# Performance work log

Hardware: AMD Instinct MI355X
Metric: run time of the kernel (lower is better)

Reference implementation:

```python
import jax, jax.numpy as jnp
import numpy as np

D_K = 64

def setup_inputs() -> dict:
    key = jax.random.key(0)
    k1, k2, k3 = jax.random.split(key, 3)
    B, H, S, d = 4, 16, 2048, D_K
    Q = jax.random.normal(k1, (B, H, S, d), dtype=jnp.float32)
    K = jax.random.normal(k2, (B, H, S, d), dtype=jnp.float32)
    V = jax.random.normal(k3, (B, H, S, d), dtype=jnp.float32)
    attn_mask = jnp.ones((1, 1, S, S), dtype=jnp.float32)
    return {"Q": Q, "K": K, "V": V, "attn_mask": attn_mask}

def reference(Q, K, V, attn_mask):
    # scores = Q K^T / sqrt(d_k)  -> [B, H, S, S]
    scale = 1.0 / np.sqrt(D_K).astype(np.float32)
    scores = jnp.einsum('bhqd,bhkd->bhqk', Q, K) * scale
    # unnormalized exp (NO max-subtraction, faithful to original)
    scores = jnp.exp(scores)
    # multiplicative mask applied POST-exp
    scores = scores * attn_mask
    # manual sum-normalization with eps
    attn = scores / (jnp.sum(scores, axis=-1, keepdims=True) + 1e-08)
    context = jnp.einsum('bhqk,bhkd->bhqd', attn, V)
    return (context, attn)
```

## Files before the change

kernel.cpp:

```cpp
#include <hip/hip_runtime.h>

#define S_LEN 2048
#define D_KD  64
#define NKT   32
#define NBH   64
#define KSEG  4

typedef __attribute__((ext_vector_type(8))) short short8;
typedef __attribute__((ext_vector_type(4))) float f32x4;

__device__ __forceinline__ unsigned short f2bf(float f) {
    unsigned u = __builtin_bit_cast(unsigned, f);
    return (unsigned short)((u + 0x7fffu + ((u >> 16) & 1u)) >> 16);
}

__device__ __forceinline__ void ldsbar() {
    asm volatile("s_waitcnt lgkmcnt(0)" ::: "memory");
    __builtin_amdgcn_s_barrier();
}

__device__ __forceinline__ unsigned swz(int row, int bytecol) {
    return (unsigned)(row * 128 + bytecol) ^
           (((((unsigned)row & 7u) ^ ((unsigned)row >> 3)) & 7u) << 4);
}

__device__ __forceinline__ void load_rm(const float* __restrict__ g,
                                        float4 r[4], int tid) {
#pragma unroll
    for (int j = 0; j < 4; j++) r[j] = *(const float4*)(g + j * 1024 + tid * 4);
}
__device__ __forceinline__ void write_rm(const float4 r[4],
                                         unsigned char* lds, int tid) {
#pragma unroll
    for (int j = 0; j < 4; j++) {
        int idx = j * 1024 + tid * 4;
        int row = idx >> 6, col = idx & 63;
        ushort4 b = make_ushort4(f2bf(r[j].x), f2bf(r[j].y), f2bf(r[j].z), f2bf(r[j].w));
        *(ushort4*)(lds + swz(row, col * 2)) = b;
    }
}
__device__ __forceinline__ void load_tr(const float* __restrict__ g,
                                        float4 r[4], int tid) {
    const int br = tid >> 4, bc = tid & 15;
    const float* gp = g + (4 * br) * 64 + 4 * bc;
#pragma unroll
    for (int j = 0; j < 4; j++) r[j] = *(const float4*)(gp + j * 64);
}
__device__ __forceinline__ void write_tr(const float4 r[4],
                                         unsigned char* lds, int tid) {
    const int br = tid >> 4, bc = tid & 15;
    ushort4 c;
    c = make_ushort4(f2bf(r[0].x), f2bf(r[1].x), f2bf(r[2].x), f2bf(r[3].x));
    *(ushort4*)(lds + swz(4 * bc + 0, 8 * br)) = c;
    c = make_ushort4(f2bf(r[0].y), f2bf(r[1].y), f2bf(r[2].y), f2bf(r[3].y));
    *(ushort4*)(lds + swz(4 * bc + 1, 8 * br)) = c;
    c = make_ushort4(f2bf(r[0].z), f2bf(r[1].z), f2bf(r[2].z), f2bf(r[3].z));
    *(ushort4*)(lds + swz(4 * bc + 2, 8 * br)) = c;
    c = make_ushort4(f2bf(r[0].w), f2bf(r[1].w), f2bf(r[2].w), f2bf(r[3].w));
    *(ushort4*)(lds + swz(4 * bc + 3, 8 * br)) = c;
}

__device__ __forceinline__ void stage_rm(const float* __restrict__ g,
                                         unsigned char* lds, int tid) {
    float4 r[4];
    load_rm(g, r, tid);
    write_rm(r, lds, tid);
}

__device__ __forceinline__ void qkt(const unsigned char* Qs, const unsigned char* Ks,
                                    int wv, int lr, int lg, f32x4 acc[4]) {
    short8 a0 = *(const short8*)(Qs + swz(16 * wv + lr, 16 * lg));
    short8 a1 = *(const short8*)(Qs + swz(16 * wv + lr, 16 * lg + 64));
#pragma unroll
    for (int nt = 0; nt < 4; nt++) {
        short8 b0 = *(const short8*)(Ks + swz(16 * nt + lr, 16 * lg));
        short8 b1 = *(const short8*)(Ks + swz(16 * nt + lr, 16 * lg + 64));
        acc[nt] = __builtin_amdgcn_mfma_f32_16x16x32_bf16(a0, b0, acc[nt], 0, 0, 0);
        acc[nt] = __builtin_amdgcn_mfma_f32_16x16x32_bf16(a1, b1, acc[nt], 0, 0, 0);
    }
}

__global__ __launch_bounds__(256) void attn_ctx(
    const float* __restrict__ Q, const float* __restrict__ K,
    const float* __restrict__ V, const float* __restrict__ M,
    float* __restrict__ out, float* __restrict__ invg) {
    __shared__ unsigned char Qs[8192];
    __shared__ unsigned char Ks[8192];
    __shared__ unsigned char Vs[8192];
    __shared__ unsigned char Ps[8192];

    const int tid = threadIdx.x;
    const int wv = tid >> 6, lane = tid & 63, lr = lane & 15, lg = lane >> 4;
    const int qt = blockIdx.x & 31, bh = blockIdx.x >> 5;

    const float* Qg = Q + ((size_t)bh * S_LEN + qt * 64) * D_KD;
    const float* Kg = K + (size_t)bh * S_LEN * D_KD;
    const float* Vg = V + (size_t)bh * S_LEN * D_KD;
    float* ctxg = out + ((size_t)bh * S_LEN + qt * 64) * D_KD;
    const float* Mg = M + (size_t)(qt * 64) * S_LEN;

    stage_rm(Qg, Qs, tid);

    f32x4 accc[4] = {};
    float rs[4] = {0.f, 0.f, 0.f, 0.f};

    float4 kreg[4], vreg[4];
    load_rm(Kg, kreg, tid);
    load_tr(Vg, vreg, tid);

    for (int t = 0; t < NKT; t++) {
        write_rm(kreg, Ks, tid);
        write_tr(vreg, Vs, tid);
        ldsbar();

        if (t + 1 < NKT) {
            load_rm(Kg + (size_t)(t + 1) * 64 * D_KD, kreg, tid);
            load_tr(Vg + (size_t)(t + 1) * 64 * D_KD, vreg, tid);
        }

        float mreg[4][4];
#pragma unroll
        for (int r = 0; r < 4; r++) {
            const float* mrow = Mg + (size_t)(16 * wv + 4 * lg + r) * S_LEN + t * 64;
#pragma unroll
            for (int nt = 0; nt < 4; nt++) mreg[r][nt] = mrow[16 * nt + lr];
        }

        f32x4 acc[4] = {};
        qkt(Qs, Ks, wv, lr, lg, acc);

#pragma unroll
        for (int r = 0; r < 4; r++) {
            const int row = 16 * wv + 4 * lg + r;
#pragma unroll
            for (int nt = 0; nt < 4; nt++) {
                float e = __expf(acc[nt][r] * 0.125f) * mreg[r][nt];
                rs[r] += e;
                *(unsigned short*)(Ps + swz(row, (16 * nt + lr) * 2)) = f2bf(e);
            }
        }
        ldsbar();

#pragma unroll
        for (int kt = 0; kt < 2; kt++) {
            short8 pa = *(const short8*)(Ps + swz(16 * wv + lr, 16 * lg + 64 * kt));
#pragma unroll
            for (int nt = 0; nt < 4; nt++) {
                short8 vb = *(const short8*)(Vs + swz(16 * nt + lr, 16 * lg + 64 * kt));
                accc[nt] = __builtin_amdgcn_mfma_f32_16x16x32_bf16(pa, vb, accc[nt], 0, 0, 0);
            }
        }
        ldsbar();
    }

    float inv[4];
#pragma unroll
    for (int r = 0; r < 4; r++) {
        float v = rs[r];
        v += __shfl_xor(v, 1);
        v += __shfl_xor(v, 2);
        v += __shfl_xor(v, 4);
        v += __shfl_xor(v, 8);
        inv[r] = 1.0f / (v + 1e-8f);
    }

#pragma unroll
    for (int r = 0; r < 4; r++) {
        const int row = 16 * wv + 4 * lg + r;
#pragma unroll
        for (int nt = 0; nt < 4; nt++)
            ctxg[(size_t)row * D_KD + 16 * nt + lr] = accc[nt][r] * inv[r];
    }

    if (lr == 0) {
#pragma unroll
        for (int r = 0; r < 4; r++)
            invg[(size_t)bh * S_LEN + qt * 64 + 16 * wv + 4 * lg + r] = inv[r];
    }
}

__global__ __launch_bounds__(256) void attn_mat(
    const float* __restrict__ Q, const float* __restrict__ K,
    const float* __restrict__ M, const float* __restrict__ invg,
    float* __restrict__ out) {
    __shared__ unsigned char Qs[8192];
    __shared__ unsigned char Ks[8192];

    const int tid = threadIdx.x;
    const int wv = tid >> 6, lane = tid & 63, lr = lane & 15, lg = lane >> 4;
    const int ks = blockIdx.x & (KSEG - 1);
    const int qt = (blockIdx.x >> 2) & 31;
    const int bh = blockIdx.x >> 7;

    const float* Qg = Q + ((size_t)bh * S_LEN + qt * 64) * D_KD;
    const float* Kg = K + (size_t)bh * S_LEN * D_KD;
    const float* Mg = M + (size_t)(qt * 64) * S_LEN;
    float* attng = out + (size_t)NBH * S_LEN * D_KD +
                   (size_t)bh * S_LEN * S_LEN + (size_t)(qt * 64) * S_LEN;

    stage_rm(Qg, Qs, tid);

    float inv[4];
#pragma unroll
    for (int r = 0; r < 4; r++)
        inv[r] = invg[(size_t)bh * S_LEN + qt * 64 + 16 * wv + 4 * lg + r];

    const int nt_kt = S_LEN / (64 * KSEG);
    const float* Kseg = Kg + (size_t)(ks * (S_LEN / KSEG)) * D_KD;

    float4 kreg[4];
    load_rm(Kseg, kreg, tid);

    for (int kt = 0; kt < nt_kt; kt++) {
        const int key0 = ks * (S_LEN / KSEG) + kt * 64;
        write_rm(kreg, Ks, tid);
        ldsbar();

        if (kt + 1 < nt_kt)
            load_rm(Kseg + (size_t)(kt + 1) * 64 * D_KD, kreg, tid);

        float mreg[4][4];
#pragma unroll
        for (int r = 0; r < 4; r++) {
            const float* mrow = Mg + (size_t)(16 * wv + 4 * lg + r) * S_LEN + key0;
#pragma unroll
            for (int nt = 0; nt < 4; nt++) mreg[r][nt] = mrow[16 * nt + lr];
        }

        f32x4 acc[4] = {};
        qkt(Qs, Ks, wv, lr, lg, acc);

#pragma unroll
        for (int r = 0; r < 4; r++) {
            const int row = 16 * wv + 4 * lg + r;
            float* arow = attng + (size_t)row * S_LEN + key0;
#pragma unroll
            for (int nt = 0; nt < 4; nt++) {
                float e = __expf(acc[nt][r] * 0.125f) * mreg[r][nt] * inv[r];
                __builtin_nontemporal_store(e, arow + 16 * nt + lr);
            }
        }
        ldsbar();
    }
}

extern "C" void kernel_launch(void* const* d_in, const int* in_sizes, int n_in,
                              void* d_out, int out_size, void* d_ws, size_t ws_size,
                              hipStream_t stream) {
    const float* Q = (const float*)d_in[0];
    const float* K = (const float*)d_in[1];
    const float* V = (const float*)d_in[2];
    const float* M = (const float*)d_in[3];
    float* out = (float*)d_out;
    float* invg = (float*)d_ws;
    attn_ctx<<<dim3(NBH * 32), dim3(256), 0, stream>>>(Q, K, V, M, out, invg);
    attn_mat<<<dim3(NBH * 32 * KSEG), dim3(256), 0, stream>>>(Q, K, M, invg, out);
}
```

Before: 461.3 us.

## Stage whole K segment up front and drop per-tile barriers in attention kernels

```diff
diff --git a/kernel.cpp b/kernel.cpp
--- a/kernel.cpp
+++ b/kernel.cpp
@@ -4,7 +4,9 @@
 #define D_KD  64
 #define NKT   32
 #define NBH   64
-#define KSEG  4
+#define KSEG  8
+#define SEGK  (S_LEN / KSEG)
+#define SEGT  (SEGK / 64)
 
 typedef __attribute__((ext_vector_type(8))) short short8;
 typedef __attribute__((ext_vector_type(4))) float f32x4;
@@ -17,6 +19,10 @@
 __device__ __forceinline__ void ldsbar() {
     asm volatile("s_waitcnt lgkmcnt(0)" ::: "memory");
     __builtin_amdgcn_s_barrier();
+}
+__device__ __forceinline__ void ldswait() {
+    asm volatile("s_waitcnt lgkmcnt(0)" ::: "memory");
+    __builtin_amdgcn_sched_barrier(0);
 }
 
 __device__ __forceinline__ unsigned swz(int row, int bytecol) {
@@ -139,7 +145,7 @@
                 *(unsigned short*)(Ps + swz(row, (16 * nt + lr) * 2)) = f2bf(e);
             }
         }
-        ldsbar();
+        ldswait();
 
 #pragma unroll
         for (int kt = 0; kt < 2; kt++) {
@@ -184,40 +190,35 @@
     const float* __restrict__ M, const float* __restrict__ invg,
     float* __restrict__ out) {
     __shared__ unsigned char Qs[8192];
-    __shared__ unsigned char Ks[8192];
+    __shared__ unsigned char Ks[SEGT * 8192];
 
     const int tid = threadIdx.x;
     const int wv = tid >> 6, lane = tid & 63, lr = lane & 15, lg = lane >> 4;
     const int ks = blockIdx.x & (KSEG - 1);
-    const int qt = (blockIdx.x >> 2) & 31;
-    const int bh = blockIdx.x >> 7;
+    const int qt = (blockIdx.x >> 3) & 31;
+    const int bh = blockIdx.x >> 8;
 
     const float* Qg = Q + ((size_t)bh * S_LEN + qt * 64) * D_KD;
-    const float* Kg = K + (size_t)bh * S_LEN * D_KD;
+    const float* Kseg = K + ((size_t)bh * S_LEN + ks * SEGK) * D_KD;
     const float* Mg = M + (size_t)(qt * 64) * S_LEN;
     float* attng = out + (size_t)NBH * S_LEN * D_KD +
                    (size_t)bh * S_LEN * S_LEN + (size_t)(qt * 64) * S_LEN;
 
     stage_rm(Qg, Qs, tid);
+#pragma unroll
+    for (int i = 0; i < SEGT; i++)
+        stage_rm(Kseg + (size_t)i * 64 * D_KD, Ks + i * 8192, tid);
 
     float inv[4];
 #pragma unroll
     for (int r = 0; r < 4; r++)
         inv[r] = invg[(size_t)bh * S_LEN + qt * 64 + 16 * wv + 4 * lg + r];
 
-    const int nt_kt = S_LEN / (64 * KSEG);
-    const float* Kseg = Kg + (size_t)(ks * (S_LEN / KSEG)) * D_KD;
-
-    float4 kreg[4];
-    load_rm(Kseg, kreg, tid);
-
-    for (int kt = 0; kt < nt_kt; kt++) {
-        const int key0 = ks * (S_LEN / KSEG) + kt * 64;
-        write_rm(kreg, Ks, tid);
-        ldsbar();
-
-        if (kt + 1 < nt_kt)
-            load_rm(Kseg + (size_t)(kt + 1) * 64 * D_KD, kreg, tid);
+    ldsbar();
+
+#pragma unroll
+    for (int kt = 0; kt < SEGT; kt++) {
+        const int key0 = ks * SEGK + kt * 64;
 
         float mreg[4][4];
 #pragma unroll
@@ -228,7 +229,7 @@
         }
 
         f32x4 acc[4] = {};
-        qkt(Qs, Ks, wv, lr, lg, acc);
+        qkt(Qs, Ks + kt * 8192, wv, lr, lg, acc);
 
 #pragma unroll
         for (int r = 0; r < 4; r++) {
@@ -240,7 +241,6 @@
                 __builtin_nontemporal_store(e, arow + 16 * nt + lr);
             }
         }
-        ldsbar();
     }
 }
 
```

After: 480.2 us. 4.1% more time.

## Enlarge ctx kernel query tile to 128 rows with register-resident Q fragments

Applied to the files above, without the earlier changes.

```diff
diff --git a/kernel.cpp b/kernel.cpp
--- a/kernel.cpp
+++ b/kernel.cpp
@@ -5,6 +5,8 @@
 #define NKT   32
 #define NBH   64
 #define KSEG  4
+#define QB1   128
+#define NQT1  (S_LEN / QB1)
 
 typedef __attribute__((ext_vector_type(8))) short short8;
 typedef __attribute__((ext_vector_type(4))) float f32x4;
@@ -13,10 +15,22 @@
     unsigned u = __builtin_bit_cast(unsigned, f);
     return (unsigned short)((u + 0x7fffu + ((u >> 16) & 1u)) >> 16);
 }
+__device__ __forceinline__ short8 pack8(float4 a, float4 b) {
+    short8 r;
+    r[0] = (short)f2bf(a.x); r[1] = (short)f2bf(a.y);
+    r[2] = (short)f2bf(a.z); r[3] = (short)f2bf(a.w);
+    r[4] = (short)f2bf(b.x); r[5] = (short)f2bf(b.y);
+    r[6] = (short)f2bf(b.z); r[7] = (short)f2bf(b.w);
+    return r;
+}
 
 __device__ __forceinline__ void ldsbar() {
     asm volatile("s_waitcnt lgkmcnt(0)" ::: "memory");
     __builtin_amdgcn_s_barrier();
+}
+__device__ __forceinline__ void ldswait() {
+    asm volatile("s_waitcnt lgkmcnt(0)" ::: "memory");
+    __builtin_amdgcn_sched_barrier(0);
 }
 
 __device__ __forceinline__ unsigned swz(int row, int bytecol) {
@@ -39,27 +53,6 @@
         *(ushort4*)(lds + swz(row, col * 2)) = b;
     }
 }
-__device__ __forceinline__ void load_tr(const float* __restrict__ g,
-                                        float4 r[4], int tid) {
-    const int br = tid >> 4, bc = tid & 15;
-    const float* gp = g + (4 * br) * 64 + 4 * bc;
-#pragma unroll
-    for (int j = 0; j < 4; j++) r[j] = *(const float4*)(gp + j * 64);
-}
-__device__ __forceinline__ void write_tr(const float4 r[4],
-                                         unsigned char* lds, int tid) {
-    const int br = tid >> 4, bc = tid & 15;
-    ushort4 c;
-    c = make_ushort4(f2bf(r[0].x), f2bf(r[1].x), f2bf(r[2].x), f2bf(r[3].x));
-    *(ushort4*)(lds + swz(4 * bc + 0, 8 * br)) = c;
-    c = make_ushort4(f2bf(r[0].y), f2bf(r[1].y), f2bf(r[2].y), f2bf(r[3].y));
-    *(ushort4*)(lds + swz(4 * bc + 1, 8 * br)) = c;
-    c = make_ushort4(f2bf(r[0].z), f2bf(r[1].z), f2bf(r[2].z), f2bf(r[3].z));
-    *(ushort4*)(lds + swz(4 * bc + 2, 8 * br)) = c;
-    c = make_ushort4(f2bf(r[0].w), f2bf(r[1].w), f2bf(r[2].w), f2bf(r[3].w));
-    *(ushort4*)(lds + swz(4 * bc + 3, 8 * br)) = c;
-}
-
 __device__ __forceinline__ void stage_rm(const float* __restrict__ g,
                                          unsigned char* lds, int tid) {
     float4 r[4];
@@ -67,6 +60,39 @@
     write_rm(r, lds, tid);
 }
 
+__device__ __forceinline__ void load_rm2(const float* __restrict__ g,
+                                         float4 r[2], int tid) {
+#pragma unroll
+    for (int j = 0; j < 2; j++) r[j] = *(const float4*)(g + j * 2048 + tid * 4);
+}
+__device__ __forceinline__ void write_rm2(const float4 r[2],
+                                          unsigned char* lds, int tid) {
+#pragma unroll
+    for (int j = 0; j < 2; j++) {
+        int idx = j * 2048 + tid * 4;
+        int row = idx >> 6, col = idx & 63;
+        ushort4 b = make_ushort4(f2bf(r[j].x), f2bf(r[j].y), f2bf(r[j].z), f2bf(r[j].w));
+        *(ushort4*)(lds + swz(row, col * 2)) = b;
+    }
+}
+__device__ __forceinline__ void load_tr2(const float* __restrict__ g,
+                                         float2 r[4], int tid) {
+    const int br = tid >> 5;
+    const int bc = tid & 31;
+    const float* gp = g + (4 * br) * 64 + 2 * bc;
+#pragma unroll
+    for (int j = 0; j < 4; j++) r[j] = *(const float2*)(gp + j * 64);
+}
+__device__ __forceinline__ void write_tr2(const float2 r[4],
+                                          unsigned char* lds, int tid) {
+    const int br = tid >> 5, bc = tid & 31;
+    ushort4 c;
+    c = make_ushort4(f2bf(r[0].x), f2bf(r[1].x), f2bf(r[2].x), f2bf(r[3].x));
+    *(ushort4*)(lds + swz(2 * bc + 0, 8 * br)) = c;
+    c = make_ushort4(f2bf(r[0].y), f2bf(r[1].y), f2bf(r[2].y), f2bf(r[3].y));
+    *(ushort4*)(lds + swz(2 * bc + 1, 8 * br)) = c;
+}
+
 __device__ __forceinline__ void qkt(const unsigned char* Qs, const unsigned char* Ks,
                                     int wv, int lr, int lg, f32x4 acc[4]) {
     short8 a0 = *(const short8*)(Qs + swz(16 * wv + lr, 16 * lg));
@@ -79,43 +105,58 @@
         acc[nt] = __builtin_amdgcn_mfma_f32_16x16x32_bf16(a1, b1, acc[nt], 0, 0, 0);
     }
 }
-
-__global__ __launch_bounds__(256) void attn_ctx(
+__device__ __forceinline__ void qkt_r(short8 qa0, short8 qa1, const unsigned char* Ks,
+                                      int lr, int lg, f32x4 acc[4]) {
+#pragma unroll
+    for (int nt = 0; nt < 4; nt++) {
+        short8 b0 = *(const short8*)(Ks + swz(16 * nt + lr, 16 * lg));
+        short8 b1 = *(const short8*)(Ks + swz(16 * nt + lr, 16 * lg + 64));
+        acc[nt] = __builtin_amdgcn_mfma_f32_16x16x32_bf16(qa0, b0, acc[nt], 0, 0, 0);
+        acc[nt] = __builtin_amdgcn_mfma_f32_16x16x32_bf16(qa1, b1, acc[nt], 0, 0, 0);
+    }
+}
+
+__global__ __launch_bounds__(512) void attn_ctx(
     const float* __restrict__ Q, const float* __restrict__ K,
     const float* __restrict__ V, const float* __restrict__ M,
     float* __restrict__ out, float* __restrict__ invg) {
-    __shared__ unsigned char Qs[8192];
     __shared__ unsigned char Ks[8192];
     __shared__ unsigned char Vs[8192];
-    __shared__ unsigned char Ps[8192];
+    __shared__ unsigned char Ps[16384];
 
     const int tid = threadIdx.x;
     const int wv = tid >> 6, lane = tid & 63, lr = lane & 15, lg = lane >> 4;
-    const int qt = blockIdx.x & 31, bh = blockIdx.x >> 5;
-
-    const float* Qg = Q + ((size_t)bh * S_LEN + qt * 64) * D_KD;
+    const int qt = blockIdx.x & (NQT1 - 1), bh = blockIdx.x >> 4;
+
+    const float* Qg = Q + ((size_t)bh * S_LEN + qt * QB1) * D_KD;
     const float* Kg = K + (size_t)bh * S_LEN * D_KD;
     const float* Vg = V + (size_t)bh * S_LEN * D_KD;
-    float* ctxg = out + ((size_t)bh * S_LEN + qt * 64) * D_KD;
-    const float* Mg = M + (size_t)(qt * 64) * S_LEN;
-
-    stage_rm(Qg, Qs, tid);
+    float* ctxg = out + ((size_t)bh * S_LEN + qt * QB1) * D_KD;
+    const float* Mg = M + (size_t)(qt * QB1) * S_LEN;
+
+    short8 qa0, qa1;
+    {
+        const float* qrow = Qg + (16 * wv + lr) * D_KD + 8 * lg;
+        qa0 = pack8(*(const float4*)(qrow), *(const float4*)(qrow + 4));
+        qa1 = pack8(*(const float4*)(qrow + 32), *(const float4*)(qrow + 36));
+    }
 
     f32x4 accc[4] = {};
     float rs[4] = {0.f, 0.f, 0.f, 0.f};
 
-    float4 kreg[4], vreg[4];
-    load_rm(Kg, kreg, tid);
-    load_tr(Vg, vreg, tid);
+    float4 kreg[2];
+    float2 vreg[4];
+    load_rm2(Kg, kreg, tid);
+    load_tr2(Vg, vreg, tid);
 
     for (int t = 0; t < NKT; t++) {
-        write_rm(kreg, Ks, tid);
-        write_tr(vreg, Vs, tid);
+        write_rm2(kreg, Ks, tid);
+        write_tr2(vreg, Vs, tid);
         ldsbar();
 
         if (t + 1 < NKT) {
-            load_rm(Kg + (size_t)(t + 1) * 64 * D_KD, kreg, tid);
-            load_tr(Vg + (size_t)(t + 1) * 64 * D_KD, vreg, tid);
+            load_rm2(Kg + (size_t)(t + 1) * 64 * D_KD, kreg, tid);
+            load_tr2(Vg + (size_t)(t + 1) * 64 * D_KD, vreg, tid);
         }
 
         float mreg[4][4];
@@ -127,7 +168,7 @@
         }
 
         f32x4 acc[4] = {};
-        qkt(Qs, Ks, wv, lr, lg, acc);
+        qkt_r(qa0, qa1, Ks, lr, lg, acc);
 
 #pragma unroll
         for (int r = 0; r < 4; r++) {
@@ -139,7 +180,7 @@
                 *(unsigned short*)(Ps + swz(row, (16 * nt + lr) * 2)) = f2bf(e);
             }
         }
-        ldsbar();
+        ldswait();
 
 #pragma unroll
         for (int kt = 0; kt < 2; kt++) {
@@ -175,7 +216,7 @@
     if (lr == 0) {
 #pragma unroll
         for (int r = 0; r < 4; r++)
-            invg[(size_t)bh * S_LEN + qt * 64 + 16 * wv + 4 * lg + r] = inv[r];
+            invg[(size_t)bh * S_LEN + qt * QB1 + 16 * wv + 4 * lg + r] = inv[r];
     }
 }
 
@@ -253,6 +294,6 @@
     const float* M = (const float*)d_in[3];
     float* out = (float*)d_out;
     float* invg = (float*)d_ws;
-    attn_ctx<<<dim3(NBH * 32), dim3(256), 0, stream>>>(Q, K, V, M, out, invg);
+    attn_ctx<<<dim3(NBH * NQT1), dim3(512), 0, stream>>>(Q, K, V, M, out, invg);
     attn_mat<<<dim3(NBH * 32 * KSEG), dim3(256), 0, stream>>>(Q, K, M, invg, out);
 }
```

After: 476.5 us. 1.03x slower.

## Load Q/K fragments directly into registers in attn_mat, drop LDS staging and barriers

Applied to the files above, without the earlier changes.

```diff
diff --git a/kernel.cpp b/kernel.cpp
--- a/kernel.cpp
+++ b/kernel.cpp
@@ -13,10 +13,22 @@
     unsigned u = __builtin_bit_cast(unsigned, f);
     return (unsigned short)((u + 0x7fffu + ((u >> 16) & 1u)) >> 16);
 }
+__device__ __forceinline__ short8 pack8(float4 a, float4 b) {
+    short8 r;
+    r[0] = (short)f2bf(a.x); r[1] = (short)f2bf(a.y);
+    r[2] = (short)f2bf(a.z); r[3] = (short)f2bf(a.w);
+    r[4] = (short)f2bf(b.x); r[5] = (short)f2bf(b.y);
+    r[6] = (short)f2bf(b.z); r[7] = (short)f2bf(b.w);
+    return r;
+}
 
 __device__ __forceinline__ void ldsbar() {
     asm volatile("s_waitcnt lgkmcnt(0)" ::: "memory");
     __builtin_amdgcn_s_barrier();
+}
+__device__ __forceinline__ void ldswait() {
+    asm volatile("s_waitcnt lgkmcnt(0)" ::: "memory");
+    __builtin_amdgcn_sched_barrier(0);
 }
 
 __device__ __forceinline__ unsigned swz(int row, int bytecol) {
@@ -59,7 +71,6 @@
     c = make_ushort4(f2bf(r[0].w), f2bf(r[1].w), f2bf(r[2].w), f2bf(r[3].w));
     *(ushort4*)(lds + swz(4 * bc + 3, 8 * br)) = c;
 }
-
 __device__ __forceinline__ void stage_rm(const float* __restrict__ g,
                                          unsigned char* lds, int tid) {
     float4 r[4];
@@ -139,7 +150,7 @@
                 *(unsigned short*)(Ps + swz(row, (16 * nt + lr) * 2)) = f2bf(e);
             }
         }
-        ldsbar();
+        ldswait();
 
 #pragma unroll
         for (int kt = 0; kt < 2; kt++) {
@@ -183,22 +194,23 @@
     const float* __restrict__ Q, const float* __restrict__ K,
     const float* __restrict__ M, const float* __restrict__ invg,
     float* __restrict__ out) {
-    __shared__ unsigned char Qs[8192];
-    __shared__ unsigned char Ks[8192];
-
     const int tid = threadIdx.x;
     const int wv = tid >> 6, lane = tid & 63, lr = lane & 15, lg = lane >> 4;
     const int ks = blockIdx.x & (KSEG - 1);
     const int qt = (blockIdx.x >> 2) & 31;
     const int bh = blockIdx.x >> 7;
 
-    const float* Qg = Q + ((size_t)bh * S_LEN + qt * 64) * D_KD;
     const float* Kg = K + (size_t)bh * S_LEN * D_KD;
     const float* Mg = M + (size_t)(qt * 64) * S_LEN;
     float* attng = out + (size_t)NBH * S_LEN * D_KD +
                    (size_t)bh * S_LEN * S_LEN + (size_t)(qt * 64) * S_LEN;
 
-    stage_rm(Qg, Qs, tid);
+    short8 qa0, qa1;
+    {
+        const float* qrow = Q + ((size_t)bh * S_LEN + qt * 64 + 16 * wv + lr) * D_KD + 8 * lg;
+        qa0 = pack8(*(const float4*)(qrow), *(const float4*)(qrow + 4));
+        qa1 = pack8(*(const float4*)(qrow + 32), *(const float4*)(qrow + 36));
+    }
 
     float inv[4];
 #pragma unroll
@@ -206,18 +218,17 @@
         inv[r] = invg[(size_t)bh * S_LEN + qt * 64 + 16 * wv + 4 * lg + r];
 
     const int nt_kt = S_LEN / (64 * KSEG);
-    const float* Kseg = Kg + (size_t)(ks * (S_LEN / KSEG)) * D_KD;
-
-    float4 kreg[4];
-    load_rm(Kseg, kreg, tid);
 
     for (int kt = 0; kt < nt_kt; kt++) {
         const int key0 = ks * (S_LEN / KSEG) + kt * 64;
-        write_rm(kreg, Ks, tid);
-        ldsbar();
-
-        if (kt + 1 < nt_kt)
-            load_rm(Kseg + (size_t)(kt + 1) * 64 * D_KD, kreg, tid);
+
+        short8 kb0[4], kb1[4];
+#pragma unroll
+        for (int nt = 0; nt < 4; nt++) {
+            const float* krow = Kg + (size_t)(key0 + 16 * nt + lr) * D_KD + 8 * lg;
+            kb0[nt] = pack8(*(const float4*)(krow), *(const float4*)(krow + 4));
+            kb1[nt] = pack8(*(const float4*)(krow + 32), *(const float4*)(krow + 36));
+        }
 
         float mreg[4][4];
 #pragma unroll
@@ -228,7 +239,11 @@
         }
 
         f32x4 acc[4] = {};
-        qkt(Qs, Ks, wv, lr, lg, acc);
+#pragma unroll
+        for (int nt = 0; nt < 4; nt++) {
+            acc[nt] = __builtin_amdgcn_mfma_f32_16x16x32_bf16(qa0, kb0[nt], acc[nt], 0, 0, 0);
+            acc[nt] = __builtin_amdgcn_mfma_f32_16x16x32_bf16(qa1, kb1[nt], acc[nt], 0, 0, 0);
+        }
 
 #pragma unroll
         for (int r = 0; r < 4; r++) {
@@ -240,7 +255,6 @@
                 __builtin_nontemporal_store(e, arow + 16 * nt + lr);
             }
         }
-        ldsbar();
     }
 }
 
```

Result: slower. 725.1 us (+57.2%).
